# Performance work log

Hardware: AMD Instinct MI355X
Metric: run time of the kernel (lower is better)

Reference implementation:

```python
import jax, jax.numpy as jnp
import numpy as np


def _conv4d(x, w, stride, pad):
    # x: [B, Cin, D1, D2, D3, D4]; w: [Cout, Cin, k, k, k, k]
    # 4D conv decomposed as a sum over the first kernel axis of strided 3D convs
    k = w.shape[2]
    if pad:
        x = jnp.pad(x, ((0, 0), (0, 0)) + ((pad, pad),) * 4)
    B, Cin, D1, D2, D3, D4 = x.shape
    o1 = (D1 - k) // stride + 1
    acc = None
    for j in range(k):  # fixed small loop over kernel taps (k<=3)
        xs = x[:, :, j:j + stride * (o1 - 1) + 1:stride]  # [B,Cin,o1,D2,D3,D4]
        xs = xs.transpose(0, 2, 1, 3, 4, 5).reshape(B * o1, Cin, D2, D3, D4)
        y = jax.lax.conv_general_dilated(
            xs, w[:, :, j], (stride,) * 3, 'VALID',
            dimension_numbers=('NCDHW', 'OIDHW', 'NCDHW'))
        acc = y if acc is None else acc + y
    Cout = w.shape[0]
    o2, o3, o4 = acc.shape[2:]
    return acc.reshape(B, o1, Cout, o2, o3, o4).transpose(0, 2, 1, 3, 4, 5)


def _cconv4d(xr, xi, wr, wi, br, bi, stride=1, pad=0):
    # complex conv: (xr+i*xi) * (wr+i*wi)
    yr = _conv4d(xr, wr, stride, pad) - _conv4d(xi, wi, stride, pad)
    yi = _conv4d(xr, wi, stride, pad) + _conv4d(xi, wr, stride, pad)
    bs = (1, -1, 1, 1, 1, 1)
    return yr + br.reshape(bs), yi + bi.reshape(bs)


def _crelu(xr, xi):
    return jax.nn.relu(xr), jax.nn.relu(xi)


def setup_inputs() -> dict:
    key = jax.random.key(0)
    ks = jax.random.split(key, 32)
    def rnd(i, shape, scale):
        return jax.random.normal(ks[i], shape, jnp.float32) * scale
    inp = {'xr': rnd(0, (4, 1, 20, 20, 20, 20), 1.0),
           'xi': rnd(1, (4, 1, 20, 20, 20, 20), 1.0)}
    specs = [(1, 32, 3), (32, 64, 3), (64, 128, 1), (128, 128, 1), (128, 64, 1)]
    i = 2
    for n, (ci, co, k) in enumerate(specs, 1):
        scale = float(1.0 / np.sqrt(ci * k ** 4))
        inp['w%dr' % n] = rnd(i, (co, ci, k, k, k, k), scale); i += 1
        inp['w%di' % n] = rnd(i, (co, ci, k, k, k, k), scale); i += 1
        inp['b%dr' % n] = rnd(i, (co,), scale); i += 1
        inp['b%di' % n] = rnd(i, (co,), scale); i += 1
    inp['fcw'] = rnd(i, (1, 625), 1.0 / 25.0); i += 1
    inp['fcb'] = rnd(i, (1,), 0.05)
    return inp


def reference(xr, xi, w1r, w1i, b1r, b1i, w2r, w2i, b2r, b2i,
              w3r, w3i, b3r, b3i, w4r, w4i, b4r, b4i,
              w5r, w5i, b5r, b5i, fcw, fcb):
    xr, xi = _crelu(*_cconv4d(xr, xi, w1r, w1i, b1r, b1i, stride=2, pad=0))  # 20->9
    xr, xi = _crelu(*_cconv4d(xr, xi, w2r, w2i, b2r, b2i, stride=1, pad=1))  # same
    xr, xi = _crelu(*_cconv4d(xr, xi, w3r, w3i, b3r, b3i))                    # 1x1
    xr, xi = _crelu(*_cconv4d(xr, xi, w4r, w4i, b4r, b4i))                    # 1x1
    xr, xi = _crelu(*_cconv4d(xr, xi, w5r, w5i, b5r, b5i, stride=2, pad=0))   # 9->5
    B = xr.shape[0]
    xr = xr.reshape(B, 64, -1)  # [B, 64, 625]
    xi = xi.reshape(B, 64, -1)
    xr, xi = _crelu(xr, xi)
    yr = xr @ fcw.T + fcb  # real bias adds to real part
    yi = xi @ fcw.T
    return jnp.stack([yr, yi])  # [2, B, 64, 1]
```

## Files before the change

### kernel.cpp

```cpp
#include <hip/hip_runtime.h>
#include <hip/hip_bf16.h>

typedef __bf16 bf16x8v __attribute__((ext_vector_type(8)));
typedef float f32x4 __attribute__((ext_vector_type(4)));

#define GLD16(gp, loff)                                                     \
  __builtin_amdgcn_global_load_lds(                                         \
      (const __attribute__((address_space(1))) void*)(gp),                  \
      (__attribute__((address_space(3))) void*)(smem + (loff)), 16, 0, 0)


__global__ __launch_bounds__(256) void prep_fused(
    const float* __restrict__ w1r, const float* __restrict__ w1i,
    const float* __restrict__ w2r, const float* __restrict__ w2i,
    const float* __restrict__ w3r, const float* __restrict__ w3i,
    const float* __restrict__ w4r, const float* __restrict__ w4i,
    const float* __restrict__ w5r, const float* __restrict__ w5i,
    __hip_bfloat16* __restrict__ w1b, __hip_bfloat16* __restrict__ wt2b,
    __hip_bfloat16* __restrict__ w3b, __hip_bfloat16* __restrict__ w4b,
    __hip_bfloat16* __restrict__ w5b, uint4* __restrict__ xpz) {
  const int bx = blockIdx.x;
  const int tid = threadIdx.x;
  auto pack11 = [](const float* wr, const float* wi, __hip_bfloat16* dst,
                   int Cout, int Cin, int idx) {
    int k2 = 2 * Cin;
    int k = idx % k2, n = idx / k2;
    int ci = (k < Cin) ? k : k - Cin;
    int co = (n < Cout) ? n : n - Cout;
    int widx = co * Cin + ci;
    float v;
    if (n < Cout) v = (k < Cin) ? wr[widx] : -wi[widx];
    else          v = (k < Cin) ? wi[widx] :  wr[widx];
    dst[idx] = __float2bfloat16(v);
  };
  if (bx < 1831) {
    int i = bx * 256 + tid;
    if (i < 468512) xpz[i] = make_uint4(0, 0, 0, 0);
  } else if (bx < 4423) {
    int idx = (bx - 1831) * 256 + tid;
    int k = idx & 63, n = (idx >> 6) & 127, t = idx >> 13;
    int ci = k & 31, kin_i = k >> 5;
    int co = n & 63, out_i = n >> 6;
    int widx = (co * 32 + ci) * 81 + t;
    float v;
    if (out_i == 0) v = (kin_i == 0) ? w2r[widx] : -w2i[widx];
    else            v = (kin_i == 0) ? w2i[widx] :  w2r[widx];
    wt2b[idx] = __float2bfloat16(v);
  } else if (bx < 4487) {
    int idx = (bx - 4423) * 256 + tid;
    int n = idx >> 8, k = idx & 255;
    int t = k >> 1, c = k & 1, co = n & 31;
    float v = 0.f;
    if (t < 81) {
      if (n < 32) v = c ? -w1i[co * 81 + t] : w1r[co * 81 + t];
      else        v = c ?  w1r[co * 81 + t] : w1i[co * 81 + t];
    }
    w1b[idx] = __float2bfloat16(v);
  } else if (bx < 4615) {
    pack11(w3r, w3i, w3b, 128, 64, (bx - 4487) * 256 + tid);
  } else if (bx < 4871) {
    pack11(w4r, w4i, w4b, 128, 128, (bx - 4615) * 256 + tid);
  } else {
    pack11(w5r, w5i, w5b, 64, 128, (bx - 4871) * 256 + tid);
  }
}

__global__ __launch_bounds__(256) void im2col_l1(
    const float* __restrict__ xr, const float* __restrict__ xi,
    __hip_bfloat16* __restrict__ Aim) {
  __shared__ uint lds[8192];
  const int tid = threadIdx.x;
  const int row = tid & 63;
  const int tg = tid >> 6;
  const int m0 = blockIdx.x * 64;
  int m = m0 + row;
  if (m > 26243) m = 26243;
  int b = m / 6561, p = m % 6561;
  int d1 = p / 729, r = p % 729;
  int d2 = r / 81;
  r %= 81;
  int d3 = r / 9, d4 = r % 9;
  const int base = b * 160000 + d1 * 16000 + d2 * 800 + d3 * 40 + d4 * 2;
  const int xorv = (row & 31) << 2;
  const int rbase = row << 7;

  const int tend = (tg == 3) ? 81 : tg * 21 + 21;
  for (int t = tg * 21; t < tend; ++t) {
    int j1 = t / 27, j2 = (t / 9) % 3, j3 = (t / 3) % 3, j4 = t % 3;
    int xo = base + j1 * 8000 + j2 * 400 + j3 * 20 + j4;
    __hip_bfloat16 h2[2] = {__float2bfloat16(xr[xo]),
                            __float2bfloat16(xi[xo])};
    lds[rbase + (t ^ xorv)] = *(const uint*)h2;
  }
  for (int t = 81 + tg; t < 128; t += 4) lds[rbase + (t ^ xorv)] = 0u;
  __syncthreads();

  uint4* dst = (uint4*)(Aim + (size_t)m0 * 256);
#pragma unroll
  for (int ph = 0; ph < 8; ++ph) {
    int W = ph * 4096 + tid * 16;
    int rw = W >> 9;
    int c4 = (W & 511) >> 2;
    int li = (rw << 7) + (c4 ^ ((rw & 31) << 2));
    uint4 v = {lds[li], lds[li + 1], lds[li + 2], lds[li + 3]};
    dst[W >> 4] = v;
  }
}

__global__ __launch_bounds__(512) void gemm_l1(
    const __hip_bfloat16* __restrict__ Aim, const __hip_bfloat16* __restrict__ Bm,
    const float* __restrict__ br, const float* __restrict__ bi,
    __hip_bfloat16* __restrict__ xp) {
  __shared__ __align__(128) char smem[65536];
  const int tid = threadIdx.x, l = tid & 63, w = tid >> 6;
  const int wm = w & 3, wn = w >> 2;
  const int p0 = blockIdx.x * 128;

  const char* aB = (const char*)Aim;
#pragma unroll
  for (int g = 0; g < 8; ++g) {
    int W = (w * 8 + g) * 1024 + (l << 4);
    int row = W >> 9;
    int cb = W & 511;
    int m = p0 + row;
    if (m > 26243) m = 26243;
    GLD16(aB + (size_t)m * 512 + (cb ^ ((row & 7) << 4)), W);
  }
  asm volatile("s_waitcnt vmcnt(0)" ::: "memory");
  __syncthreads();

  const int l15 = l & 15;
  const int klo = (l >> 4) << 4;
  const int sx = (l & 7) << 4;
  const int arow0 = (wm * 32 + l15) * 512;
  const char* bb = (const char*)Bm + (size_t)(wn * 32 + l15) * 512 + klo;

  f32x4 acc[2][2];
#pragma unroll
  for (int mi = 0; mi < 2; ++mi)
#pragma unroll
    for (int ni = 0; ni < 2; ++ni) acc[mi][ni] = (f32x4){0.f, 0.f, 0.f, 0.f};

#pragma unroll
  for (int kh = 0; kh < 8; ++kh) {
    bf16x8v bfr[2];
#pragma unroll
    for (int ni = 0; ni < 2; ++ni)
      bfr[ni] = *(const bf16x8v*)(bb + ni * 16 * 512 + kh * 64);
    const int kx = ((kh << 6) + klo) ^ sx;
    bf16x8v af[2];
#pragma unroll
    for (int mi = 0; mi < 2; ++mi)
      af[mi] = *(const bf16x8v*)(smem + arow0 + mi * 8192 + kx);
#pragma unroll
    for (int mi = 0; mi < 2; ++mi)
#pragma unroll
      for (int ni = 0; ni < 2; ++ni)
        acc[mi][ni] = __builtin_amdgcn_mfma_f32_16x16x32_bf16(
            af[mi], bfr[ni], acc[mi][ni], 0, 0, 0);
  }

  const int prow = p0 + wm * 32 + ((l >> 4) << 2);
  const int col0 = wn * 32 + l15;
#pragma unroll
  for (int ni = 0; ni < 2; ++ni) {
    int cn = col0 + ni * 16;
    float bias = (cn < 32) ? br[cn] : bi[cn - 32];
#pragma unroll
    for (int mi = 0; mi < 2; ++mi)
#pragma unroll
      for (int j = 0; j < 4; ++j) {
        int m = prow + mi * 16 + j;
        if (m < 26244) {
          int b = m / 6561, p = m % 6561;
          int d1 = p / 729, r = p % 729;
          int d2 = r / 81;
          r %= 81;
          int d3 = r / 9, d4 = r % 9;
          int q = (((d1 + 1) * 11 + (d2 + 1)) * 11 + (d3 + 1)) * 11 + (d4 + 1);
          xp[((size_t)(b * 14641 + q)) * 64 + cn] =
              __float2bfloat16(fmaxf(acc[mi][ni][j] + bias, 0.f));
        }
      }
  }
}

__global__ __launch_bounds__(256) void cconv2_ksplit(
    const __hip_bfloat16* __restrict__ xp, const __hip_bfloat16* __restrict__ wb,
    __hip_bfloat16* __restrict__ part) {
  __shared__ __align__(128) char smem[65536];
  const int tid = threadIdx.x;
  const int l = tid & 63, w = tid >> 6;
  const int wm = w & 1, wn = w >> 1;
  const int m0 = blockIdx.x * 128;
  const int ky = blockIdx.y;

  const int swz = ((l & 7) ^ (l >> 3)) << 4;
  const char* xpB = (const char*)xp;
  const char* wB = (const char*)wb;
  int q00[4], rbB[4];
#pragma unroll
  for (int c = 0; c < 4; ++c) {
    int row = w * 32 + c * 8 + (l >> 3);
    int m = m0 + row;
    if (m > 26243) m = 26243;
    int b = m / 6561, p = m % 6561;
    int d1 = p / 729, r = p % 729;
    int d2 = r / 81;
    r %= 81;
    int d3 = r / 9, d4 = r % 9;
    q00[c] = b * 14641 + ((d1 * 11 + d2) * 11 + d3) * 11 + d4;
    rbB[c] = row * 128 + swz;
  }

  const int l15 = l & 15;
  const int klo = (l >> 4) << 4;
  const int sx = (l & 7) << 4;
  const int arow0 = (wm * 64 + l15) * 128;
  const int brow0 = 16384 + (wn * 64 + l15) * 128;

  f32x4 acc[4][4];
#pragma unroll
  for (int mi = 0; mi < 4; ++mi)
#pragma unroll
    for (int ni = 0; ni < 4; ++ni) acc[mi][ni] = (f32x4){0.f, 0.f, 0.f, 0.f};

  auto stage = [&](int t, int nb) {
    int j1 = t / 27, j2 = (t / 9) % 3, j3 = (t / 3) % 3, j4 = t % 3;
    int delta = ((j1 * 11 + j2) * 11 + j3) * 11 + j4;
#pragma unroll
    for (int c = 0; c < 4; ++c) {
      GLD16(xpB + (((size_t)(q00[c] + delta)) << 7) + swz,
            nb + w * 4096 + c * 1024);
      GLD16(wB + (((size_t)t) << 14) + rbB[c],
            nb + 16384 + w * 4096 + c * 1024);
    }
  };

  const int t0 = ky * 41;
  const int nt = 41 - ky;

  stage(t0, 0);

  for (int ti = 0; ti < nt; ++ti) {
    asm volatile("s_waitcnt vmcnt(0)" ::: "memory");
    __builtin_amdgcn_s_barrier();
    if (ti + 1 < nt) stage(t0 + ti + 1, ((ti + 1) & 1) * 32768);
    const char* sb = smem + (ti & 1) * 32768;
#pragma unroll
    for (int kh = 0; kh < 2; ++kh) {
      const int kx = ((kh << 6) + klo) ^ sx;
      bf16x8v af[4], bfr[4];
#pragma unroll
      for (int mi = 0; mi < 4; ++mi)
        af[mi] = *(const bf16x8v*)(sb + arow0 + mi * 2048 + kx);
#pragma unroll
      for (int ni = 0; ni < 4; ++ni)
        bfr[ni] = *(const bf16x8v*)(sb + brow0 + ni * 2048 + kx);
#pragma unroll
      for (int mi = 0; mi < 4; ++mi)
#pragma unroll
        for (int ni = 0; ni < 4; ++ni)
          acc[mi][ni] = __builtin_amdgcn_mfma_f32_16x16x32_bf16(
              af[mi], bfr[ni], acc[mi][ni], 0, 0, 0);
    }
  }

  __hip_bfloat16* pp = part + (size_t)ky * 3359232;
  const int prow = m0 + wm * 64 + ((l >> 4) << 2);
  const int col0 = wn * 64 + l15;
#pragma unroll
  for (int ni = 0; ni < 4; ++ni) {
    int cn = col0 + ni * 16;
#pragma unroll
    for (int mi = 0; mi < 4; ++mi)
#pragma unroll
      for (int j = 0; j < 4; ++j) {
        int m = prow + mi * 16 + j;
        if (m < 26244)
          pp[(size_t)m * 128 + cn] = __float2bfloat16(acc[mi][ni][j]);
      }
  }
}

__global__ __launch_bounds__(512) void gemm_fused34(
    const __hip_bfloat16* __restrict__ p0, const __hip_bfloat16* __restrict__ p1,
    const __hip_bfloat16* __restrict__ w3, const __hip_bfloat16* __restrict__ w4,
    const float* __restrict__ b2r, const float* __restrict__ b2i,
    const float* __restrict__ b3r, const float* __restrict__ b3i,
    const float* __restrict__ b4r, const float* __restrict__ b4i,
    __hip_bfloat16* __restrict__ a4) {
  __shared__ __align__(128) char smem[98304];
  const int tid = threadIdx.x, l = tid & 63, w = tid >> 6;
  const int wm = w & 1, wn = w >> 1;
  const int pfix = blockIdx.x * 128;

  {
    int r = tid >> 2;
    int cb = (tid & 3) * 32;
    int m = pfix + r;
    if (m > 26243) m = 26243;
    const uint2* q0 = (const uint2*)(p0 + (size_t)m * 128 + cb);
    const uint2* q1 = (const uint2*)(p1 + (size_t)m * 128 + cb);
    __hip_bfloat16 tmp[32];
#pragma unroll
    for (int i = 0; i < 8; ++i) {
      uint2 ua = q0[i], ub = q1[i];
      const __hip_bfloat16* a = (const __hip_bfloat16*)&ua;
      const __hip_bfloat16* b = (const __hip_bfloat16*)&ub;
#pragma unroll
      for (int e = 0; e < 4; ++e) {
        int cn = cb + i * 4 + e;
        float bias = (cn < 64) ? b2r[cn] : b2i[cn - 64];
        float s = __bfloat162float(a[e]) + __bfloat162float(b[e]) + bias;
        tmp[i * 4 + e] = __float2bfloat16(fmaxf(s, 0.f));
      }
    }
    const int rs = (r & 7) << 4;
#pragma unroll
    for (int s4 = 0; s4 < 4; ++s4) {
      int col = cb * 2 + s4 * 16;
      *(uint4*)(smem + r * 256 + (col ^ rs)) = ((const uint4*)tmp)[s4];
    }
  }
  __syncthreads();

  const int l15 = l & 15;
  const int klo = (l >> 4) << 4;
  const int sx = (l & 7) << 4;

  f32x4 acc[4][4];
#pragma unroll
  for (int mi = 0; mi < 4; ++mi)
#pragma unroll
    for (int ni = 0; ni < 4; ++ni) acc[mi][ni] = (f32x4){0.f, 0.f, 0.f, 0.f};

  {
    const int arow3 = (wm * 64 + l15) * 256;
    const char* b3b = (const char*)w3 + (size_t)(wn * 64 + l15) * 256 + klo;
#pragma unroll
    for (int kh = 0; kh < 4; ++kh) {
      const int kx = ((kh << 6) + klo) ^ sx;
      bf16x8v af[4], bfr[4];
#pragma unroll
      for (int mi = 0; mi < 4; ++mi)
        af[mi] = *(const bf16x8v*)(smem + arow3 + mi * 4096 + kx);
#pragma unroll
      for (int ni = 0; ni < 4; ++ni)
        bfr[ni] = *(const bf16x8v*)(b3b + ni * 4096 + kh * 64);
#pragma unroll
      for (int mi = 0; mi < 4; ++mi)
#pragma unroll
        for (int ni = 0; ni < 4; ++ni)
          acc[mi][ni] = __builtin_amdgcn_mfma_f32_16x16x32_bf16(
              af[mi], bfr[ni], acc[mi][ni], 0, 0, 0);
    }
  }

  __syncthreads();
  {
    const int lrow = wm * 64 + ((l >> 4) << 2);
    const int col0 = wn * 64 + l15;
#pragma unroll
    for (int ni = 0; ni < 4; ++ni) {
      int cn = col0 + ni * 16;
      float bias = (cn < 128) ? b3r[cn] : b3i[cn - 128];
#pragma unroll
      for (int mi = 0; mi < 4; ++mi) {
        int row = lrow + mi * 16;
#pragma unroll
        for (int j = 0; j < 4; ++j) {
          float v = fmaxf(acc[mi][ni][j] + bias, 0.f);
          int addr = (32768 + (row + j) * 512 + cn * 2) ^ (((row + j) & 7) << 4);
          *(__hip_bfloat16*)(smem + addr) = __float2bfloat16(v);
        }
      }
    }
  }
  __syncthreads();

#pragma unroll
  for (int mi = 0; mi < 4; ++mi)
#pragma unroll
    for (int ni = 0; ni < 4; ++ni) acc[mi][ni] = (f32x4){0.f, 0.f, 0.f, 0.f};
  {
    const int arow4 = 32768 + (wm * 64 + l15) * 512;
    const char* b4b = (const char*)w4 + (size_t)(wn * 64 + l15) * 512 + klo;
#pragma unroll
    for (int kh = 0; kh < 8; ++kh) {
      const int kx = ((kh << 6) + klo) ^ sx;
      bf16x8v af[4], bfr[4];
#pragma unroll
      for (int mi = 0; mi < 4; ++mi)
        af[mi] = *(const bf16x8v*)(smem + arow4 + mi * 8192 + kx);
#pragma unroll
      for (int ni = 0; ni < 4; ++ni)
        bfr[ni] = *(const bf16x8v*)(b4b + ni * 8192 + kh * 64);
#pragma unroll
      for (int mi = 0; mi < 4; ++mi)
#pragma unroll
        for (int ni = 0; ni < 4; ++ni)
          acc[mi][ni] = __builtin_amdgcn_mfma_f32_16x16x32_bf16(
              af[mi], bfr[ni], acc[mi][ni], 0, 0, 0);
    }
  }

  {
    const int prow = pfix + wm * 64 + ((l >> 4) << 2);
    const int col0 = wn * 64 + l15;
#pragma unroll
    for (int ni = 0; ni < 4; ++ni) {
      int cn = col0 + ni * 16;
      float bias = (cn < 128) ? b4r[cn] : b4i[cn - 128];
#pragma unroll
      for (int mi = 0; mi < 4; ++mi)
#pragma unroll
        for (int j = 0; j < 4; ++j) {
          int m = prow + mi * 16 + j;
          if (m < 26244)
            a4[(size_t)m * 256 + cn] =
                __float2bfloat16(fmaxf(acc[mi][ni][j] + bias, 0.f));
        }
    }
  }
}

template <int K, int S2>
__global__ __launch_bounds__(512) void gemm_bg(
    const __hip_bfloat16* __restrict__ A, const __hip_bfloat16* __restrict__ Bm,
    const float* __restrict__ br, const float* __restrict__ bi,
    __hip_bfloat16* __restrict__ C, int M, int N, int Cout) {
  constexpr int ROWB = 2 * K;
  constexpr int NKH = K / 32;
  constexpr int LG = (K == 128) ? 8 : 9;
  __shared__ __align__(128) char smem[128 * ROWB];
  const int tid = threadIdx.x, l = tid & 63, w = tid >> 6;
  const int wm = w & 1, wn = w >> 1;
  const int p0 = blockIdx.x * 128, n0 = blockIdx.y * 128;

  const char* aB = (const char*)A;
#pragma unroll
  for (int g = 0; g < NKH; ++g) {
    int W = (w * NKH + g) * 1024 + (l << 4);
    int row = W >> LG;
    int cb = W & (ROWB - 1);
    int m = p0 + row;
    if (m >= M) m = M - 1;
    int srcrow;
    if (S2) {
      int bb_ = m / 625, r = m % 625;
      int d1 = r / 125;
      r %= 125;
      int d2 = r / 25;
      r %= 25;
      int d3 = r / 5, d4 = r % 5;
      srcrow = bb_ * 6561 + d1 * 1458 + d2 * 162 + d3 * 18 + d4 * 2;
    } else {
      srcrow = m;
    }
    GLD16(aB + (size_t)srcrow * ROWB + (cb ^ ((row & 7) << 4)), W);
  }
  asm volatile("s_waitcnt vmcnt(0)" ::: "memory");
  __syncthreads();

  const int l15 = l & 15;
  const int klo = (l >> 4) << 4;
  const int sx = (l & 7) << 4;
  const int arow0 = (wm * 64 + l15) * ROWB;
  const char* bb = (const char*)Bm + (size_t)(n0 + wn * 32 + l15) * ROWB + klo;

  f32x4 acc[4][2];
#pragma unroll
  for (int mi = 0; mi < 4; ++mi)
#pragma unroll
    for (int ni = 0; ni < 2; ++ni) acc[mi][ni] = (f32x4){0.f, 0.f, 0.f, 0.f};

#pragma unroll
  for (int kh = 0; kh < NKH; ++kh) {
    bf16x8v bfr[2];
#pragma unroll
    for (int ni = 0; ni < 2; ++ni)
      bfr[ni] = *(const bf16x8v*)(bb + ni * 16 * ROWB + kh * 64);
    const int kx = ((kh << 6) + klo) ^ sx;
    bf16x8v af[4];
#pragma unroll
    for (int mi = 0; mi < 4; ++mi)
      af[mi] = *(const bf16x8v*)(smem + arow0 + mi * 16 * ROWB + kx);
#pragma unroll
    for (int mi = 0; mi < 4; ++mi)
#pragma unroll
      for (int ni = 0; ni < 2; ++ni)
        acc[mi][ni] = __builtin_amdgcn_mfma_f32_16x16x32_bf16(
            af[mi], bfr[ni], acc[mi][ni], 0, 0, 0);
  }

  const int prow = p0 + wm * 64 + ((l >> 4) << 2);
  const int col0 = n0 + wn * 32 + l15;
#pragma unroll
  for (int ni = 0; ni < 2; ++ni) {
    int cn = col0 + ni * 16;
    float bias = (cn < Cout) ? br[cn] : bi[cn - Cout];
#pragma unroll
    for (int mi = 0; mi < 4; ++mi)
#pragma unroll
      for (int j = 0; j < 4; ++j) {
        int m = prow + mi * 16 + j;
        if (m < M)
          C[(size_t)m * N + cn] =
              __float2bfloat16(fmaxf(acc[mi][ni][j] + bias, 0.f));
      }
  }
}

__global__ __launch_bounds__(256) void fc_kernel(
    const __hip_bfloat16* __restrict__ a5, const float* __restrict__ fcw,
    const float* __restrict__ fcb, float* __restrict__ out) {
  int bc = blockIdx.x * 4 + (threadIdx.x >> 6);
  int b = bc >> 6, c = bc & 63;
  int lane = threadIdx.x & 63;
  const __hip_bfloat16* base = a5 + (size_t)b * 625 * 128;
  float sr = 0.f, si = 0.f;
  for (int p = lane; p < 625; p += 64) {
    float wv = fcw[p];
    sr += __bfloat162float(base[(size_t)p * 128 + c]) * wv;
    si += __bfloat162float(base[(size_t)p * 128 + 64 + c]) * wv;
  }
#pragma unroll
  for (int s = 32; s > 0; s >>= 1) {
    sr += __shfl_down(sr, s);
    si += __shfl_down(si, s);
  }
  if (lane == 0) {
    out[bc] = sr + fcb[0];
    out[256 + bc] = si;
  }
}

extern "C" void kernel_launch(void* const* d_in, const int* in_sizes, int n_in,
                              void* d_out, int out_size, void* d_ws,
                              size_t ws_size, hipStream_t stream) {
  const float* xr = (const float*)d_in[0];
  const float* xi = (const float*)d_in[1];
  const float* w1r = (const float*)d_in[2];
  const float* w1i = (const float*)d_in[3];
  const float* b1r = (const float*)d_in[4];
  const float* b1i = (const float*)d_in[5];
  const float* w2r = (const float*)d_in[6];
  const float* w2i = (const float*)d_in[7];
  const float* b2r = (const float*)d_in[8];
  const float* b2i = (const float*)d_in[9];
  const float* w3r = (const float*)d_in[10];
  const float* w3i = (const float*)d_in[11];
  const float* b3r = (const float*)d_in[12];
  const float* b3i = (const float*)d_in[13];
  const float* w4r = (const float*)d_in[14];
  const float* w4i = (const float*)d_in[15];
  const float* b4r = (const float*)d_in[16];
  const float* b4i = (const float*)d_in[17];
  const float* w5r = (const float*)d_in[18];
  const float* w5i = (const float*)d_in[19];
  const float* b5r = (const float*)d_in[20];
  const float* b5i = (const float*)d_in[21];
  const float* fcw = (const float*)d_in[22];
  const float* fcb = (const float*)d_in[23];
  float* out = (float*)d_out;

  float* ws = (float*)d_ws;
  __hip_bfloat16* wt2b = (__hip_bfloat16*)(ws + 5184);
  __hip_bfloat16* w3b = (__hip_bfloat16*)(ws + 336960);
  __hip_bfloat16* w4b = (__hip_bfloat16*)(ws + 353344);
  __hip_bfloat16* w5b = (__hip_bfloat16*)(ws + 386112);
  __hip_bfloat16* xp = (__hip_bfloat16*)(ws + 402496);
  __hip_bfloat16* a4 = (__hip_bfloat16*)(ws + 3956160);
  __hip_bfloat16* a5 = (__hip_bfloat16*)(ws + 7315392);
  __hip_bfloat16* w1b = (__hip_bfloat16*)(ws + 7475392);
  __hip_bfloat16* part = (__hip_bfloat16*)(ws + 7483584);
  __hip_bfloat16* Aim = (__hip_bfloat16*)(ws + 3956160);

  prep_fused<<<dim3(4999), 256, 0, stream>>>(
      w1r, w1i, w2r, w2i, w3r, w3i, w4r, w4i, w5r, w5i, w1b, wt2b, w3b, w4b,
      w5b, (uint4*)xp);

  im2col_l1<<<dim3(411), 256, 0, stream>>>(xr, xi, Aim);
  gemm_l1<<<dim3(206), 512, 0, stream>>>(Aim, w1b, b1r, b1i, xp);
  cconv2_ksplit<<<dim3(206, 2), 256, 0, stream>>>(xp, wt2b, part);
  gemm_fused34<<<dim3(206), 512, 0, stream>>>(
      part, part + 3359232, w3b, w4b, b2r, b2i, b3r, b3i, b4r, b4i, a4);
  gemm_bg<256, 1><<<dim3(20, 1), 512, 0, stream>>>(a4, w5b, b5r, b5i, a5,
                                                   2500, 128, 64);
  fc_kernel<<<dim3(64), 256, 0, stream>>>(a5, fcw, fcb, out);
}
```

Before: 112.8 us.

## Fuse im2col into prep kernel, zero only halo, stage gemm_l1 epilogue in LDS

Merges the layer-1 im2col into the weight-prep kernel as extra blocks, which removes one launch. The padded activation buffer now has only its halo zeroed, since the interior is fully written by gemm_l1 later. The gemm_l1 epilogue writes results into LDS with a swizzle, then emits 16-byte coalesced row stores instead of scattered 2-byte stores. The cost is extra syncs, and the prep kernel now statically allocates 32KB of LDS for every block, which may lower occupancy for the weight-pack blocks.

```diff
diff --git a/kernel.cpp b/kernel.cpp
--- a/kernel.cpp
+++ b/kernel.cpp
@@ -11,6 +11,7 @@
 
 
 __global__ __launch_bounds__(256) void prep_fused(
+    const float* __restrict__ xr, const float* __restrict__ xi,
     const float* __restrict__ w1r, const float* __restrict__ w1i,
     const float* __restrict__ w2r, const float* __restrict__ w2i,
     const float* __restrict__ w3r, const float* __restrict__ w3i,
@@ -18,7 +19,9 @@
     const float* __restrict__ w5r, const float* __restrict__ w5i,
     __hip_bfloat16* __restrict__ w1b, __hip_bfloat16* __restrict__ wt2b,
     __hip_bfloat16* __restrict__ w3b, __hip_bfloat16* __restrict__ w4b,
-    __hip_bfloat16* __restrict__ w5b, uint4* __restrict__ xpz) {
+    __hip_bfloat16* __restrict__ w5b, uint4* __restrict__ xpz,
+    __hip_bfloat16* __restrict__ Aim) {
+  __shared__ uint lds[8192];
   const int bx = blockIdx.x;
   const int tid = threadIdx.x;
   auto pack11 = [](const float* wr, const float* wi, __hip_bfloat16* dst,
@@ -35,7 +38,18 @@
   };
   if (bx < 1831) {
     int i = bx * 256 + tid;
-    if (i < 468512) xpz[i] = make_uint4(0, 0, 0, 0);
+    if (i < 468512) {
+      int q = (i >> 3) % 14641;
+      unsigned e4 = q % 11;
+      int r_ = q / 11;
+      unsigned e3 = r_ % 11;
+      r_ /= 11;
+      unsigned e2 = r_ % 11;
+      unsigned e1 = r_ / 11;
+      bool interior = (e1 - 1u) < 9u && (e2 - 1u) < 9u && (e3 - 1u) < 9u &&
+                      (e4 - 1u) < 9u;
+      if (!interior) xpz[i] = make_uint4(0, 0, 0, 0);
+    }
   } else if (bx < 4423) {
     int idx = (bx - 1831) * 256 + tid;
     int k = idx & 63, n = (idx >> 6) & 127, t = idx >> 13;
@@ -60,50 +74,44 @@
     pack11(w3r, w3i, w3b, 128, 64, (bx - 4487) * 256 + tid);
   } else if (bx < 4871) {
     pack11(w4r, w4i, w4b, 128, 128, (bx - 4615) * 256 + tid);
+  } else if (bx < 4999) {
+    pack11(w5r, w5i, w5b, 64, 128, (bx - 4871) * 256 + tid);
   } else {
-    pack11(w5r, w5i, w5b, 64, 128, (bx - 4871) * 256 + tid);
-  }
-}
-
-__global__ __launch_bounds__(256) void im2col_l1(
-    const float* __restrict__ xr, const float* __restrict__ xi,
-    __hip_bfloat16* __restrict__ Aim) {
-  __shared__ uint lds[8192];
-  const int tid = threadIdx.x;
-  const int row = tid & 63;
-  const int tg = tid >> 6;
-  const int m0 = blockIdx.x * 64;
-  int m = m0 + row;
-  if (m > 26243) m = 26243;
-  int b = m / 6561, p = m % 6561;
-  int d1 = p / 729, r = p % 729;
-  int d2 = r / 81;
-  r %= 81;
-  int d3 = r / 9, d4 = r % 9;
-  const int base = b * 160000 + d1 * 16000 + d2 * 800 + d3 * 40 + d4 * 2;
-  const int xorv = (row & 31) << 2;
-  const int rbase = row << 7;
-
-  const int tend = (tg == 3) ? 81 : tg * 21 + 21;
-  for (int t = tg * 21; t < tend; ++t) {
-    int j1 = t / 27, j2 = (t / 9) % 3, j3 = (t / 3) % 3, j4 = t % 3;
-    int xo = base + j1 * 8000 + j2 * 400 + j3 * 20 + j4;
-    __hip_bfloat16 h2[2] = {__float2bfloat16(xr[xo]),
-                            __float2bfloat16(xi[xo])};
-    lds[rbase + (t ^ xorv)] = *(const uint*)h2;
-  }
-  for (int t = 81 + tg; t < 128; t += 4) lds[rbase + (t ^ xorv)] = 0u;
-  __syncthreads();
-
-  uint4* dst = (uint4*)(Aim + (size_t)m0 * 256);
-#pragma unroll
-  for (int ph = 0; ph < 8; ++ph) {
-    int W = ph * 4096 + tid * 16;
-    int rw = W >> 9;
-    int c4 = (W & 511) >> 2;
-    int li = (rw << 7) + (c4 ^ ((rw & 31) << 2));
-    uint4 v = {lds[li], lds[li + 1], lds[li + 2], lds[li + 3]};
-    dst[W >> 4] = v;
+    const int row = tid & 63;
+    const int tg = tid >> 6;
+    const int m0 = (bx - 4999) * 64;
+    int m = m0 + row;
+    if (m > 26243) m = 26243;
+    int b = m / 6561, p = m % 6561;
+    int d1 = p / 729, r = p % 729;
+    int d2 = r / 81;
+    r %= 81;
+    int d3 = r / 9, d4 = r % 9;
+    const int base = b * 160000 + d1 * 16000 + d2 * 800 + d3 * 40 + d4 * 2;
+    const int xorv = (row & 31) << 2;
+    const int rbase = row << 7;
+
+    const int tend = (tg == 3) ? 81 : tg * 21 + 21;
+    for (int t = tg * 21; t < tend; ++t) {
+      int j1 = t / 27, j2 = (t / 9) % 3, j3 = (t / 3) % 3, j4 = t % 3;
+      int xo = base + j1 * 8000 + j2 * 400 + j3 * 20 + j4;
+      __hip_bfloat16 h2[2] = {__float2bfloat16(xr[xo]),
+                              __float2bfloat16(xi[xo])};
+      lds[rbase + (t ^ xorv)] = *(const uint*)h2;
+    }
+    for (int t = 81 + tg; t < 128; t += 4) lds[rbase + (t ^ xorv)] = 0u;
+    __syncthreads();
+
+    uint4* dst = (uint4*)(Aim + (size_t)m0 * 256);
+#pragma unroll
+    for (int ph = 0; ph < 8; ++ph) {
+      int W = ph * 4096 + tid * 16;
+      int rw = W >> 9;
+      int c4 = (W & 511) >> 2;
+      int li = (rw << 7) + (c4 ^ ((rw & 31) << 2));
+      uint4 v = {lds[li], lds[li + 1], lds[li + 2], lds[li + 3]};
+      dst[W >> 4] = v;
+    }
   }
 }
 
@@ -160,28 +168,43 @@
             af[mi], bfr[ni], acc[mi][ni], 0, 0, 0);
   }
 
-  const int prow = p0 + wm * 32 + ((l >> 4) << 2);
-  const int col0 = wn * 32 + l15;
-#pragma unroll
-  for (int ni = 0; ni < 2; ++ni) {
-    int cn = col0 + ni * 16;
-    float bias = (cn < 32) ? br[cn] : bi[cn - 32];
-#pragma unroll
-    for (int mi = 0; mi < 2; ++mi)
-#pragma unroll
-      for (int j = 0; j < 4; ++j) {
-        int m = prow + mi * 16 + j;
-        if (m < 26244) {
-          int b = m / 6561, p = m % 6561;
-          int d1 = p / 729, r = p % 729;
-          int d2 = r / 81;
-          r %= 81;
-          int d3 = r / 9, d4 = r % 9;
-          int q = (((d1 + 1) * 11 + (d2 + 1)) * 11 + (d3 + 1)) * 11 + (d4 + 1);
-          xp[((size_t)(b * 14641 + q)) * 64 + cn] =
+  __syncthreads();
+  {
+    const int lrow0 = wm * 32 + ((l >> 4) << 2);
+    const int ch0 = wn * 32 + l15;
+#pragma unroll
+    for (int ni = 0; ni < 2; ++ni) {
+      int ch = ch0 + ni * 16;
+      float bias = (ch < 32) ? br[ch] : bi[ch - 32];
+#pragma unroll
+      for (int mi = 0; mi < 2; ++mi)
+#pragma unroll
+        for (int j = 0; j < 4; ++j) {
+          int row = lrow0 + mi * 16 + j;
+          int byteoff =
+              row * 128 + ((((ch >> 3) ^ (row & 7)) << 4)) + (ch & 7) * 2;
+          *(__hip_bfloat16*)(smem + byteoff) =
               __float2bfloat16(fmaxf(acc[mi][ni][j] + bias, 0.f));
         }
-      }
+    }
+  }
+  __syncthreads();
+#pragma unroll
+  for (int it = 0; it < 2; ++it) {
+    int W = it * 8192 + tid * 16;
+    int row = W >> 7;
+    int slot = (W & 127) >> 4;
+    int m = p0 + row;
+    if (m < 26244) {
+      uint4 v = *(const uint4*)(smem + row * 128 + ((slot ^ (row & 7)) << 4));
+      int b = m / 6561, p = m % 6561;
+      int d1 = p / 729, r = p % 729;
+      int d2 = r / 81;
+      r %= 81;
+      int d3 = r / 9, d4 = r % 9;
+      int q = (((d1 + 1) * 11 + (d2 + 1)) * 11 + (d3 + 1)) * 11 + (d4 + 1);
+      *(uint4*)(xp + ((size_t)(b * 14641 + q)) * 64 + slot * 8) = v;
+    }
   }
 }
 
@@ -577,11 +600,10 @@
   __hip_bfloat16* part = (__hip_bfloat16*)(ws + 7483584);
   __hip_bfloat16* Aim = (__hip_bfloat16*)(ws + 3956160);
 
-  prep_fused<<<dim3(4999), 256, 0, stream>>>(
-      w1r, w1i, w2r, w2i, w3r, w3i, w4r, w4i, w5r, w5i, w1b, wt2b, w3b, w4b,
-      w5b, (uint4*)xp);
-
-  im2col_l1<<<dim3(411), 256, 0, stream>>>(xr, xi, Aim);
+  prep_fused<<<dim3(5410), 256, 0, stream>>>(
+      xr, xi, w1r, w1i, w2r, w2i, w3r, w3i, w4r, w4i, w5r, w5i, w1b, wt2b,
+      w3b, w4b, w5b, (uint4*)xp, Aim);
+
   gemm_l1<<<dim3(206), 512, 0, stream>>>(Aim, w1b, b1r, b1i, xp);
   cconv2_ksplit<<<dim3(206, 2), 256, 0, stream>>>(xp, wt2b, part);
   gemm_fused34<<<dim3(206), 512, 0, stream>>>(
```

Result: faster. 108.5 us (-3.8%).
